# Performance work log

Measured on AMD Instinct MI355X. Metric: run time of the kernel, lower is better.

Reference implementation:

```python
import jax, jax.numpy as jnp
import numpy as np

B, S, D, H = 32, 512, 512, 8
DF = D // H  # dim_feature = 64
NEG_INF = -1e32


def setup_inputs() -> dict:
    key = jax.random.key(0)
    ks = jax.random.split(key, 8)
    std = 1.0 / np.sqrt(D)  # xavier-ish scale for square linears
    return {
        "q": jax.random.normal(ks[0], (B, S, D), jnp.float32),
        "k": jax.random.normal(ks[1], (B, S, D), jnp.float32),
        "v": jax.random.normal(ks[2], (B, S, D), jnp.float32),
        "mask": jnp.tril(jnp.ones((S, S), jnp.int32))[None, None],  # causal AKT mask
        "zero_pad": 1,
        "question_difficulty_emb": jax.random.normal(ks[3], (B, S, S), jnp.float32) * 0.1,
        "Wk": jax.random.normal(ks[4], (D, D), jnp.float32) * std,
        "bk": jnp.zeros((D,), jnp.float32),
        "Wv": jax.random.normal(ks[5], (D, D), jnp.float32) * std,
        "bv": jnp.zeros((D,), jnp.float32),
        "Wo": jax.random.normal(ks[6], (D, D), jnp.float32) * std,
        "bo": jnp.zeros((D,), jnp.float32),
        "gammas": jax.random.normal(ks[7], (H, 1, 1), jnp.float32) * 0.1,
    }


def reference(q, k, v, mask, zero_pad, question_difficulty_emb, Wk, bk, Wv, bv, Wo, bo, gammas):
    bs = q.shape[0]

    def proj(x, W, b):
        # Linear then split heads: [B,S,D] -> [B,H,S,DF]
        return (x @ W.T + b).reshape(bs, -1, H, DF).transpose(0, 2, 1, 3)

    qh = proj(q, Wk, bk)  # key_query_same=True: q uses key_linear
    kh = proj(k, Wk, bk)
    vh = proj(v, Wv, bv)

    scores = jnp.einsum("bhqd,bhkd->bhqk", qh, kh) / jnp.sqrt(jnp.float32(DF))
    seqlen = scores.shape[-1]
    maskb = mask == 0  # [1,1,S,S]

    # --- distance-decay term (computed under no_grad in torch, detached) ---
    scores_ = jax.nn.softmax(jnp.where(maskb, NEG_INF, scores), axis=-1)
    scores_ = scores_ * mask.astype(scores.dtype)
    distcum = jnp.cumsum(scores_, axis=-1)                      # [B,H,S,S]
    disttot = jnp.sum(scores_, axis=-1, keepdims=True)          # [B,H,S,1]
    pos = jnp.abs(jnp.arange(seqlen)[None, :] - jnp.arange(seqlen)[:, None]).astype(scores.dtype)
    dist_scores = jnp.sqrt(jnp.clip((disttot - distcum) * pos[None, None], 0.0))
    dist_scores = jax.lax.stop_gradient(dist_scores)

    gamma = -jax.nn.softplus(gammas)[None]                      # [1,H,1,1]
    diff = jnp.exp(jax.nn.sigmoid(question_difficulty_emb))[:, None]  # [B,1,S,S]
    total_effect = jnp.clip(jnp.exp(dist_scores * gamma * diff), 1e-5, 1e5)

    scores = scores * total_effect
    scores = jax.nn.softmax(jnp.where(maskb, NEG_INF, scores), axis=-1)
    if zero_pad:
        scores = scores.at[:, :, 0, :].set(0.0)  # zero first query row
    scores = jnp.where(maskb, 0.0, scores)
    # dropout p=0 (eval) -> identity

    out = jnp.einsum("bhqk,bhkd->bhqd", scores, vh)
    concat = out.transpose(0, 2, 1, 3).reshape(bs, -1, D)
    return concat @ Wo.T + bo
```

## Files before the change

kernel.cpp:

```cpp
#include <hip/hip_runtime.h>

typedef unsigned short u16;
typedef __attribute__((ext_vector_type(8))) short short8;
typedef __attribute__((ext_vector_type(8))) _Float16 h8;
typedef __attribute__((ext_vector_type(4))) float f32x4;

__device__ __forceinline__ float b2f(u16 u) {
    return __uint_as_float(((unsigned int)u) << 16);
}
__device__ __forceinline__ u16 f2b(float f) {
    unsigned int x = __float_as_uint(f);
    return (u16)((x + 0x7FFFu + ((x >> 16) & 1u)) >> 16);
}
__device__ __forceinline__ float ldf(const void* p, size_t i, bool f32) {
    return f32 ? ((const float*)p)[i] : b2f(((const u16*)p)[i]);
}
__device__ __forceinline__ void stf(void* p, size_t i, bool f32, float v) {
    if (f32) ((float*)p)[i] = v; else ((u16*)p)[i] = f2b(v);
}

__device__ __forceinline__ void ldsld16(const void* g, void* l) {
    __builtin_amdgcn_global_load_lds(
        (const __attribute__((address_space(1))) unsigned int*)g,
        (__attribute__((address_space(3))) unsigned int*)l, 16, 0, 0);
}

__global__ void detect_f32(const u16* __restrict__ q, int* __restrict__ flag) {
    __shared__ int cw, cz;
    if (threadIdx.x == 0) { cw = 0; cz = 0; }
    __syncthreads();
    int w = 0, z = 0;
    for (int i = threadIdx.x; i < 4096; i += 256) {
        u16 u = q[i];
        int e = (u >> 7) & 0xFF;
        if (e >= 0xC8) w++;
        if (((i & 1) == 0) && u == 0) z++;
    }
    atomicAdd(&cw, w); atomicAdd(&cz, z);
    __syncthreads();
    if (threadIdx.x == 0) *flag = (cw > 8 || cz > 1024) ? 1 : 0;
}

__global__ __launch_bounds__(256) void cvt3(
    const void* __restrict__ s0, const void* __restrict__ s1,
    const void* __restrict__ s2, u16* __restrict__ d0, u16* __restrict__ d1,
    u16* __restrict__ d2, int n, const int* __restrict__ flag)
{
    const bool f32 = (*flag) != 0;
    const int z = blockIdx.z;
    const void* src = (z == 0) ? s0 : (z == 1) ? s1 : s2;
    u16* dst = (z == 0) ? d0 : (z == 1) ? d1 : d2;
    const int i = (blockIdx.x * 256 + threadIdx.x) * 8;
    if (i >= n) return;
    short8 o;
    if (f32) {
        const float4* s = (const float4*)((const float*)src + i);
        float4 v0 = s[0], v1 = s[1];
        o[0] = (short)f2b(v0.x); o[1] = (short)f2b(v0.y);
        o[2] = (short)f2b(v0.z); o[3] = (short)f2b(v0.w);
        o[4] = (short)f2b(v1.x); o[5] = (short)f2b(v1.y);
        o[6] = (short)f2b(v1.z); o[7] = (short)f2b(v1.w);
    } else {
        o = *(const short8*)((const u16*)src + i);
    }
    *(short8*)(dst + i) = o;
}

#define BM 128
#define BN 128
#define BK 32

__device__ __forceinline__ void gemm_body(
    const u16* __restrict__ A, const u16* __restrict__ W,
    const void* __restrict__ bias, void* __restrict__ dst,
    bool f32, int mode, int bm, int bn, int M, int N, int K)
{
    __shared__ u16 As[BM * BK];
    __shared__ u16 Bs[BN * BK];
    const int t = threadIdx.x;
    const int w = t >> 6, l = t & 63, lq = l & 15, quad = l >> 4;
    const int wr = (w >> 1) * 64, wc = (w & 1) * 64;

    const int whalf = (w & 1) * 64;
    const u16* gsrc = (w < 2) ? A : W;
    const int  gbase = (w < 2) ? bm : bn;
    u16* lbase = (w < 2) ? As : Bs;

    f32x4 acc[4][4] = {};

    for (int k0 = 0; k0 < K; k0 += BK) {
        __syncthreads();
        #pragma unroll
        for (int c = 0; c < 4; ++c) {
            const int row = whalf + c * 16 + (l >> 2);
            ldsld16(gsrc + (size_t)(gbase + row) * K + k0 + (l & 3) * 8,
                    lbase + row * BK + (l & 3) * 8);
        }
        asm volatile("s_waitcnt vmcnt(0)" ::: "memory");
        __syncthreads();
        short8 af[4], bf[4];
        #pragma unroll
        for (int i = 0; i < 4; ++i)
            af[i] = *(const short8*)&As[(wr + i * 16 + lq) * BK + quad * 8];
        #pragma unroll
        for (int j = 0; j < 4; ++j)
            bf[j] = *(const short8*)&Bs[(wc + j * 16 + lq) * BK + quad * 8];
        #pragma unroll
        for (int i = 0; i < 4; ++i)
            #pragma unroll
            for (int j = 0; j < 4; ++j)
                acc[i][j] = __builtin_amdgcn_mfma_f32_16x16x32_bf16(
                    af[i], bf[j], acc[i][j], 0, 0, 0);
    }

    #pragma unroll
    for (int j = 0; j < 4; ++j) {
        const int n = bn + wc + j * 16 + lq;
        const float bb = ldf(bias, n, f32);
        #pragma unroll
        for (int i = 0; i < 4; ++i) {
            #pragma unroll
            for (int r = 0; r < 4; ++r) {
                const int m = bm + wr + i * 16 + quad * 4 + r;
                const float vout = acc[i][j][r] + bb;
                if (mode == 0) {
                    const int b = m >> 9, s = m & 511, hh = n >> 6, df = n & 63;
                    ((u16*)dst)[((((size_t)b * 8 + hh) * 512 + s) << 6) + df] = f2b(vout);
                } else if (mode == 2) {
                    const int b = m >> 9, s = m & 511, hh = n >> 6, df = n & 63;
                    ((u16*)dst)[((((size_t)b * 8 + hh) * 64 + df) << 9) + s] = f2b(vout);
                } else {
                    stf(dst, (size_t)m * N + n, f32, vout);
                }
            }
        }
    }
}

__global__ __launch_bounds__(256) void proj3(
    const u16* __restrict__ cq, const u16* __restrict__ ck,
    const u16* __restrict__ cv, const u16* __restrict__ cWk,
    const u16* __restrict__ cWv, const void* __restrict__ bk,
    const void* __restrict__ bv, u16* __restrict__ qh, u16* __restrict__ kh,
    u16* __restrict__ vt, const int* __restrict__ flag, int M, int N, int K)
{
    const int z = blockIdx.z;
    const u16* A = (z == 0) ? cq : (z == 1) ? ck : cv;
    const u16* W = (z < 2) ? cWk : cWv;
    const void* bias = (z < 2) ? bk : bv;
    void* dst = (z == 0) ? (void*)qh : (z == 1) ? (void*)kh : (void*)vt;
    gemm_body(A, W, bias, dst, (*flag) != 0, (z < 2) ? 0 : 2,
              blockIdx.y * BM, blockIdx.x * BN, M, N, K);
}

__global__ __launch_bounds__(256) void gemm_out(
    const u16* __restrict__ A, const u16* __restrict__ W,
    const void* __restrict__ bias, void* __restrict__ dst,
    const int* __restrict__ flag, int M, int N, int K)
{
    gemm_body(A, W, bias, dst, (*flag) != 0, 1,
              blockIdx.y * BM, blockIdx.x * BN, M, N, K);
}

#define QT  16
#define SRS 568
#define PRS 584

__global__ __launch_bounds__(512) void akt_attn(
    const u16* __restrict__ qh, const u16* __restrict__ kh,
    const u16* __restrict__ vt, const void* __restrict__ qde,
    const void* __restrict__ gammas, const int* __restrict__ zero_pad,
    const int* __restrict__ flag, u16* __restrict__ attn)
{
    __shared__ _Float16 s_h[QT * SRS];
    __shared__ u16      p_lds[QT * PRS];

    const int blk = blockIdx.x;
    const int h = blk & 7;
    const int i0 = blk >> 3;
    const int qt = i0 & 31;
    const int b = i0 >> 5;

    const int q0 = qt * QT;
    const int t = threadIdx.x, w = t >> 6, l = t & 63;
    const int lq = l & 15, quad = l >> 4;
    const bool f32 = (*flag) != 0;
    const size_t bh = ((size_t)b * 8 + h) * 512;
    const int qmax = q0 + QT - 1;

    {
        const u16* qb = qh + (bh + q0) * 64;
        short8 af0 = *(const short8*)(qb + lq * 64 +      quad * 8);
        short8 af1 = *(const short8*)(qb + lq * 64 + 32 + quad * 8);
        const u16* kb = kh + bh * 64;
        const int KT = (q0 + QT + 127) >> 7;
        int n0 = w * 16;
        bool act = (n0 <= qmax);
        short8 bf0, bf1;
        if (act) {
            bf0 = *(const short8*)(kb + (size_t)(n0 + lq) * 64 +      quad * 8);
            bf1 = *(const short8*)(kb + (size_t)(n0 + lq) * 64 + 32 + quad * 8);
        }
        for (int kt = 0; kt < KT; ++kt) {
            const int n0n = (kt + 1) * 128 + w * 16;
            const bool actn = (kt + 1 < KT) && (n0n <= qmax);
            short8 nb0, nb1;
            if (actn) {
                nb0 = *(const short8*)(kb + (size_t)(n0n + lq) * 64 +      quad * 8);
                nb1 = *(const short8*)(kb + (size_t)(n0n + lq) * 64 + 32 + quad * 8);
            }
            if (act) {
                f32x4 acc = {0.f, 0.f, 0.f, 0.f};
                acc = __builtin_amdgcn_mfma_f32_16x16x32_bf16(af0, bf0, acc, 0, 0, 0);
                acc = __builtin_amdgcn_mfma_f32_16x16x32_bf16(af1, bf1, acc, 0, 0, 0);
                const int cm = n0 + lq + 8 * (n0 >> 6);
                #pragma unroll
                for (int r = 0; r < 4; ++r)
                    s_h[(quad * 4 + r) * SRS + cm] = (_Float16)(acc[r] * 0.125f);
            }
            bf0 = nb0; bf1 = nb1; act = actn; n0 = n0n;
        }
    }
    __syncthreads();

    {
        const float gma = -log1pf(expf(ldf(gammas, h, f32)));
        const int zp = zero_pad[0];
        const int c0 = l * 8;
        #pragma unroll
        for (int rr = 0; rr < 2; ++rr) {
            const int row = w * 2 + rr;
            const int q = q0 + row;
            float x[8];
            const size_t qoff = ((size_t)b * 512 + q) * 512 + c0;
            if (f32) {
                const float4* qp = (const float4*)((const float*)qde + qoff);
                float4 x0 = qp[0], x1 = qp[1];
                x[0] = x0.x; x[1] = x0.y; x[2] = x0.z; x[3] = x0.w;
                x[4] = x1.x; x[5] = x1.y; x[6] = x1.z; x[7] = x1.w;
            } else {
                short8 v8 = *(const short8*)((const u16*)qde + qoff);
                #pragma unroll
                for (int j = 0; j < 8; ++j) x[j] = b2f((u16)v8[j]);
            }
            h8 sv = *(const h8*)(s_h + row * SRS + l * 8 + 8 * (l >> 3));
            float s[8];
            #pragma unroll
            for (int j = 0; j < 8; ++j)
                s[j] = (c0 + j <= q) ? (float)sv[j] : -1e30f;
            float cs[8]; float run = 0.f;
            #pragma unroll
            for (int j = 0; j < 8; ++j) { float p = __expf(s[j]); run += p; cs[j] = run; }
            float incl = run;
            #pragma unroll
            for (int o = 1; o < 64; o <<= 1) {
                float u = __shfl_up(incl, o, 64);
                if (l >= o) incl += u;
            }
            const float ls   = __shfl(incl, 63, 64);
            const float inv1 = __builtin_amdgcn_rcpf(ls);
            const float exclr = incl - run;
            float f8[8]; float lf = 0.f;
            #pragma unroll
            for (int j = 0; j < 8; ++j) {
                float dc   = (exclr + cs[j]) * inv1;
                float rem  = 1.f - dc;
                float pos  = (float)(q - (c0 + j));
                float dist = __builtin_amdgcn_sqrtf(fmaxf(rem * pos, 0.f));
                float sig  = __builtin_amdgcn_rcpf(1.f + __expf(-x[j]));
                float eff  = __expf(dist * gma * __expf(sig));
                eff = fminf(fmaxf(eff, 1e-5f), 1e5f);
                float s2 = (c0 + j <= q) ? s[j] * eff : -1e30f;
                float f = __expf(s2);
                f8[j] = f; lf += f;
            }
            #pragma unroll
            for (int o = 32; o > 0; o >>= 1) lf += __shfl_xor(lf, o, 64);
            float inv2 = __builtin_amdgcn_rcpf(lf);
            if (zp && q == 0) inv2 = 0.f;
            short8 pb;
            #pragma unroll
            for (int j = 0; j < 8; ++j) pb[j] = (short)f2b(f8[j] * inv2);
            *(short8*)(p_lds + row * PRS + c0 + 8 * (l >> 3)) = pb;
        }
    }
    __syncthreads();

    {
        const int g = w & 3;
        const int half = w >> 2;
        const int KS = (qmax >> 5) + 1;
        const u16* vb = vt + ((size_t)(b * 8 + h) * 64 + g * 16 + lq) * 512;
        const u16* prow = p_lds + lq * PRS;
        f32x4 oacc = {0.f, 0.f, 0.f, 0.f};
        for (int ks = half; ks < KS; ks += 2) {
            const int kb2 = ks * 32 + quad * 8;
            short8 pa = *(const short8*)(prow + kb2 + 8 * (kb2 >> 6));
            short8 vv = *(const short8*)(vb + kb2);
            oacc = __builtin_amdgcn_mfma_f32_16x16x32_bf16(pa, vv, oacc, 0, 0, 0);
        }
        float* opart = (float*)s_h;
        if (half == 1) {
            #pragma unroll
            for (int r = 0; r < 4; ++r)
                opart[(g * 16 + quad * 4 + r) * 17 + lq] = oacc[r];
        }
        __syncthreads();
        if (half == 0) {
            const size_t ob = ((size_t)b * 512 + q0 + quad * 4) * 512 + h * 64 + g * 16 + lq;
            #pragma unroll
            for (int r = 0; r < 4; ++r)
                attn[ob + (size_t)r * 512] =
                    f2b(oacc[r] + opart[(g * 16 + quad * 4 + r) * 17 + lq]);
        }
    }
}

extern "C" void kernel_launch(void* const* d_in, const int* in_sizes, int n_in,
                              void* d_out, int out_size, void* d_ws, size_t ws_size,
                              hipStream_t stream) {
    const void* q   = d_in[0];
    const void* k   = d_in[1];
    const void* v   = d_in[2];
    const int*  zp  = (const int*)d_in[4];
    const void* qde = d_in[5];
    const void* Wk  = d_in[6];
    const void* bk  = d_in[7];
    const void* Wv  = d_in[8];
    const void* bv  = d_in[9];
    const void* Wo  = d_in[10];
    const void* bo  = d_in[11];
    const void* gam = d_in[12];

    const int M = 32 * 512, N = 512, K = 512;
    const int NBIG = M * K;
    const int NW = 512 * 512;

    char* ws = (char*)d_ws;
    int* flag = (int*)ws;
    const size_t SZB = (size_t)NBIG * 2;
    const size_t SZW = (size_t)NW * 2;
    u16* cWk  = (u16*)(ws + 1024);
    u16* cWv  = (u16*)(ws + 1024 + SZW);
    u16* cWo  = (u16*)(ws + 1024 + 2 * SZW);
    u16* cq   = (u16*)(ws + 1024 + 3 * SZW);
    u16* ck   = (u16*)(ws + 1024 + 3 * SZW + SZB);
    u16* cv   = (u16*)(ws + 1024 + 3 * SZW + 2 * SZB);
    u16* qh   = (u16*)(ws + 1024 + 3 * SZW + 3 * SZB);
    u16* kh   = (u16*)(ws + 1024 + 3 * SZW + 4 * SZB);
    u16* vt   = (u16*)(ws + 1024 + 3 * SZW + 5 * SZB);
    u16* attn = (u16*)(ws + 1024 + 3 * SZW + 6 * SZB);

    detect_f32<<<1, 256, 0, stream>>>((const u16*)q, flag);
    cvt3<<<dim3(NW / 2048, 1, 3), 256, 0, stream>>>(Wk, Wv, Wo, cWk, cWv, cWo, NW, flag);
    cvt3<<<dim3(NBIG / 2048, 1, 3), 256, 0, stream>>>(q, k, v, cq, ck, cv, NBIG, flag);
    proj3<<<dim3(N / BN, M / BM, 3), 256, 0, stream>>>(
        cq, ck, cv, cWk, cWv, bk, bv, qh, kh, vt, flag, M, N, K);
    akt_attn<<<8192, 512, 0, stream>>>(qh, kh, vt, qde, gam, zp, flag, attn);
    gemm_out<<<dim3(N / BN, M / BM), 256, 0, stream>>>(attn, cWo, bo, d_out, flag, M, N, K);
}
```

Measured before the change: 386.3 us.

## Precompute difficulty factor in a separate kernel and use base-2 exponentials

A new prep_diff kernel computes exp(sigmoid(qde)) once into an fp16 buffer, reusing the cq workspace after projection. The attention kernel then reads that buffer instead of the raw qde and drops its per-element sigmoid and exp. Scores are pre-scaled by log2(e), gamma is folded likewise, and exponentials use v_exp_f32 (base 2) directly. The first clamp is applied in the log domain, the upper clamp is dropped, and the suffix-sum arithmetic is simplified. This costs an extra kernel launch plus an fp16 round-trip of the difficulty tensor, which slightly reduces its precision.

```diff
diff --git a/kernel.cpp b/kernel.cpp
--- a/kernel.cpp
+++ b/kernel.cpp
@@ -17,6 +17,9 @@
 }
 __device__ __forceinline__ void stf(void* p, size_t i, bool f32, float v) {
     if (f32) ((float*)p)[i] = v; else ((u16*)p)[i] = f2b(v);
+}
+__device__ __forceinline__ float ex2(float x) {
+    float r; asm("v_exp_f32 %0, %1" : "=v"(r) : "v"(x)); return r;
 }
 
 __device__ __forceinline__ void ldsld16(const void* g, void* l) {
@@ -66,6 +69,33 @@
     *(short8*)(dst + i) = o;
 }
 
+__global__ __launch_bounds__(256) void prep_diff(
+    const void* __restrict__ qde, _Float16* __restrict__ diff, int n,
+    const int* __restrict__ flag)
+{
+    const bool f32 = (*flag) != 0;
+    const int i = (blockIdx.x * 256 + threadIdx.x) * 8;
+    if (i >= n) return;
+    float x[8];
+    if (f32) {
+        const float4* s = (const float4*)((const float*)qde + i);
+        float4 v0 = s[0], v1 = s[1];
+        x[0] = v0.x; x[1] = v0.y; x[2] = v0.z; x[3] = v0.w;
+        x[4] = v1.x; x[5] = v1.y; x[6] = v1.z; x[7] = v1.w;
+    } else {
+        short8 v8 = *(const short8*)((const u16*)qde + i);
+        #pragma unroll
+        for (int j = 0; j < 8; ++j) x[j] = b2f((u16)v8[j]);
+    }
+    h8 o;
+    #pragma unroll
+    for (int j = 0; j < 8; ++j) {
+        float sig = __builtin_amdgcn_rcpf(1.f + __expf(-x[j]));
+        o[j] = (_Float16)__expf(sig);
+    }
+    *(h8*)(diff + i) = o;
+}
+
 #define BM 128
 #define BN 128
 #define BK 32
@@ -168,7 +198,7 @@
 
 __global__ __launch_bounds__(512) void akt_attn(
     const u16* __restrict__ qh, const u16* __restrict__ kh,
-    const u16* __restrict__ vt, const void* __restrict__ qde,
+    const u16* __restrict__ vt, const _Float16* __restrict__ diff,
     const void* __restrict__ gammas, const int* __restrict__ zero_pad,
     const int* __restrict__ flag, u16* __restrict__ attn)
 {
@@ -216,7 +246,8 @@
                 const int cm = n0 + lq + 8 * (n0 >> 6);
                 #pragma unroll
                 for (int r = 0; r < 4; ++r)
-                    s_h[(quad * 4 + r) * SRS + cm] = (_Float16)(acc[r] * 0.125f);
+                    s_h[(quad * 4 + r) * SRS + cm] =
+                        (_Float16)(acc[r] * 0.180336880f);
             }
             bf0 = nb0; bf1 = nb1; act = actn; n0 = n0n;
         }
@@ -224,33 +255,26 @@
     __syncthreads();
 
     {
-        const float gma = -log1pf(expf(ldf(gammas, h, f32)));
+        const float g = ldf(gammas, h, f32);
+        const float gl2 = -log1pf(expf(g)) * 1.4426950408889634f;
         const int zp = zero_pad[0];
         const int c0 = l * 8;
         #pragma unroll
         for (int rr = 0; rr < 2; ++rr) {
             const int row = w * 2 + rr;
             const int q = q0 + row;
-            float x[8];
             const size_t qoff = ((size_t)b * 512 + q) * 512 + c0;
-            if (f32) {
-                const float4* qp = (const float4*)((const float*)qde + qoff);
-                float4 x0 = qp[0], x1 = qp[1];
-                x[0] = x0.x; x[1] = x0.y; x[2] = x0.z; x[3] = x0.w;
-                x[4] = x1.x; x[5] = x1.y; x[6] = x1.z; x[7] = x1.w;
-            } else {
-                short8 v8 = *(const short8*)((const u16*)qde + qoff);
-                #pragma unroll
-                for (int j = 0; j < 8; ++j) x[j] = b2f((u16)v8[j]);
-            }
-            h8 sv = *(const h8*)(s_h + row * SRS + l * 8 + 8 * (l >> 3));
-            float s[8];
-            #pragma unroll
-            for (int j = 0; j < 8; ++j)
-                s[j] = (c0 + j <= q) ? (float)sv[j] : -1e30f;
-            float cs[8]; float run = 0.f;
-            #pragma unroll
-            for (int j = 0; j < 8; ++j) { float p = __expf(s[j]); run += p; cs[j] = run; }
+            h8 dv = *(const h8*)(diff + qoff);
+            h8 sv16 = *(const h8*)(s_h + row * SRS + c0 + 8 * (l >> 3));
+            float sv[8], cs[8];
+            float run = 0.f;
+            #pragma unroll
+            for (int j = 0; j < 8; ++j) {
+                float s = (c0 + j <= q) ? (float)sv16[j] : -1e30f;
+                sv[j] = s;
+                float p = ex2(s);
+                run += p; cs[j] = run;
+            }
             float incl = run;
             #pragma unroll
             for (int o = 1; o < 64; o <<= 1) {
@@ -259,19 +283,18 @@
             }
             const float ls   = __shfl(incl, 63, 64);
             const float inv1 = __builtin_amdgcn_rcpf(ls);
-            const float exclr = incl - run;
+            const float t0   = ls - incl + run;
+            const float qf   = (float)(q - c0);
             float f8[8]; float lf = 0.f;
             #pragma unroll
             for (int j = 0; j < 8; ++j) {
-                float dc   = (exclr + cs[j]) * inv1;
-                float rem  = 1.f - dc;
-                float pos  = (float)(q - (c0 + j));
-                float dist = __builtin_amdgcn_sqrtf(fmaxf(rem * pos, 0.f));
-                float sig  = __builtin_amdgcn_rcpf(1.f + __expf(-x[j]));
-                float eff  = __expf(dist * gma * __expf(sig));
-                eff = fminf(fmaxf(eff, 1e-5f), 1e5f);
-                float s2 = (c0 + j <= q) ? s[j] * eff : -1e30f;
-                float f = __expf(s2);
+                float suf  = t0 - cs[j];
+                float pos  = qf - (float)j;
+                float m    = fmaxf(suf * pos, 0.f) * inv1;
+                float dist = __builtin_amdgcn_sqrtf(m);
+                float a    = fmaxf(dist * gl2 * (float)dv[j], -16.609640474f);
+                float eff  = ex2(a);
+                float f    = ex2(sv[j] * eff);
                 f8[j] = f; lf += f;
             }
             #pragma unroll
@@ -356,6 +379,8 @@
     cvt3<<<dim3(NBIG / 2048, 1, 3), 256, 0, stream>>>(q, k, v, cq, ck, cv, NBIG, flag);
     proj3<<<dim3(N / BN, M / BM, 3), 256, 0, stream>>>(
         cq, ck, cv, cWk, cWv, bk, bv, qh, kh, vt, flag, M, N, K);
-    akt_attn<<<8192, 512, 0, stream>>>(qh, kh, vt, qde, gam, zp, flag, attn);
+    _Float16* diffb = (_Float16*)cq;
+    prep_diff<<<dim3(NBIG / 2048), 256, 0, stream>>>(qde, diffb, NBIG, flag);
+    akt_attn<<<8192, 512, 0, stream>>>(qh, kh, vt, diffb, gam, zp, flag, attn);
     gemm_out<<<dim3(N / BN, M / BM), 256, 0, stream>>>(attn, cWo, bo, d_out, flag, M, N, K);
 }
```

Measured after the change: 394.1 us. +2.0%, slower.
